# Kernel optimization log

Hardware: AMD Instinct MI355X
Metric: run time of the kernel (lower is better)

The kernel has to match this reference:

```python
import jax, jax.numpy as jnp
import numpy as np

GROUP_SIZE = 64
SCALING = 1.0  # lora_alpha / r = 16 / 16
# bitsandbytes NF4 codebook (16 normal-float levels)
NF4_CODE = jnp.array([
    -1.0, -0.6961928009986877, -0.5250730514526367, -0.39491748809814453,
    -0.28444138169288635, -0.18477343022823334, -0.09105003625154495, 0.0,
    0.07958029955625534, 0.16093020141124725, 0.24611230194568634,
    0.33791524171829224, 0.44070982933044434, 0.5626170039176941,
    0.7229568362236023, 1.0], dtype=jnp.float32)

IN_F, OUT_F, R, TOKENS = 4096, 11008, 16, 32


def setup_inputs() -> dict:
    key = jax.random.key(0)
    k0, k1, k2, k3, k4 = jax.random.split(key, 5)
    x = jax.random.normal(k0, (TOKENS, IN_F), dtype=jnp.float32)
    # each byte packs two 4-bit NF4 indices (high nibble first)
    packed_weight = jax.random.randint(k1, (OUT_F * IN_F // 2,), 0, 256, dtype=jnp.int32)
    # per-group absmax scales (positive)
    scales = jax.random.uniform(k2, (OUT_F * IN_F // GROUP_SIZE,), dtype=jnp.float32,
                                minval=0.005, maxval=0.05)
    lora_A = jax.random.normal(k3, (R, IN_F), dtype=jnp.float32) * 0.02
    lora_B = jax.random.normal(k4, (OUT_F, R), dtype=jnp.float32) * 0.02
    return {"x": x, "packed_weight": packed_weight, "scales": scales,
            "lora_A": lora_A, "lora_B": lora_B}


def _dequant_nf4(packed_weight, scales):
    hi = packed_weight // 16          # first nibble
    lo = packed_weight % 16           # second nibble
    idx = jnp.stack([hi, lo], axis=-1).reshape(-1)          # [out*in]
    w = NF4_CODE[idx].reshape(-1, GROUP_SIZE) * scales[:, None]
    return w.reshape(OUT_F, IN_F)                            # [out, in]


def reference(x, packed_weight, scales, lora_A, lora_B):
    W = _dequant_nf4(packed_weight, scales)
    base = x @ W.T                                           # [tokens, out]
    lora = (x @ lora_A.T) @ lora_B.T                         # low-rank update
    return base + SCALING * lora
```

## Files before the change

kernel.cpp:

```cpp
#include <hip/hip_runtime.h>
#include <hip/hip_bf16.h>

#define IN_F 4096
#define OUT_F 11008
#define TOKENS 32
#define RANK 16
#define KSPLIT 8
#define KSLICE (IN_F / KSPLIT)

typedef unsigned short u16;
typedef __attribute__((ext_vector_type(8))) short bf16x8;
typedef __attribute__((ext_vector_type(4))) float f32x4;

__device__ const float NF4_d[16] = {
    -1.0f, -0.6961928009986877f, -0.5250730514526367f, -0.39491748809814453f,
    -0.28444138169288635f, -0.18477343022823334f, -0.09105003625154495f, 0.0f,
    0.07958029955625534f, 0.16093020141124725f, 0.24611230194568634f,
    0.33791524171829224f, 0.44070982933044434f, 0.5626170039176941f,
    0.7229568362236023f, 1.0f};

static __device__ __forceinline__ unsigned pk2(float a, float b) {
    __hip_bfloat162 h = __float22bfloat162_rn(make_float2(a, b));
    unsigned u;
    __builtin_memcpy(&u, &h, 4);
    return u;
}

__global__ void cvt_x(const float* __restrict__ x, u16* __restrict__ xbf) {
    int i4 = blockIdx.x * 256 + threadIdx.x;
    float4 v = ((const float4*)x)[i4];
    uint2 o;
    o.x = pk2(v.x, v.y);
    o.y = pk2(v.z, v.w);
    ((uint2*)xbf)[i4] = o;
}

__global__ void lora_xa(const float* __restrict__ x, const float* __restrict__ A,
                        float* __restrict__ xa) {
    int b = blockIdx.x;
    int t = b >> 4, r = b & 15;
    const float4* xr = (const float4*)(x + t * IN_F);
    const float4* ar = (const float4*)(A + r * IN_F);
    float s = 0.f;
    for (int c = 0; c < 4; ++c) {
        int j = c * 256 + threadIdx.x;
        float4 xv = xr[j], av = ar[j];
        s += xv.x * av.x + xv.y * av.y + xv.z * av.z + xv.w * av.w;
    }
    __shared__ float red[256];
    red[threadIdx.x] = s;
    __syncthreads();
    for (int st = 128; st > 0; st >>= 1) {
        if (threadIdx.x < st) red[threadIdx.x] += red[threadIdx.x + st];
        __syncthreads();
    }
    if (threadIdx.x == 0) xa[b] = red[0];
}

__global__ void lora_out(const float* __restrict__ xa, const float* __restrict__ B,
                         float* __restrict__ out) {
    int idx = blockIdx.x * 256 + threadIdx.x;
    int t = idx / OUT_F;
    int o = idx - t * OUT_F;
    const float4* br = (const float4*)(B + o * RANK);
    const float4* xr = (const float4*)(xa + t * RANK);
    float acc = 0.f;
    for (int c = 0; c < 4; ++c) {
        float4 bv = br[c], xv = xr[c];
        acc += bv.x * xv.x + bv.y * xv.y + bv.z * xv.z + bv.w * xv.w;
    }
    out[idx] = acc;
}

__global__ __launch_bounds__(256) void qlora_main(const int* __restrict__ packed,
                                                  const float* __restrict__ scales,
                                                  const u16* __restrict__ xbf,
                                                  float* __restrict__ out) {
    __shared__ u16 xs[32 * 520];
    __shared__ float2 tbl[256];
    const int tid = threadIdx.x;
    const int kbase = blockIdx.y * KSLICE;

    tbl[tid] = make_float2(NF4_d[tid >> 4], NF4_d[tid & 15]);

    for (int it = 0; it < 8; ++it) {
        int row = it * 4 + (tid >> 6);
        int c8 = tid & 63;
        const uint4* src = (const uint4*)(xbf + row * IN_F + kbase + c8 * 8);
        *(uint4*)(xs + row * 520 + c8 * 8) = *src;
    }
    __syncthreads();

    const int lane = tid & 63;
    const int wv = tid >> 6;
    const int n = lane & 15;
    const int q = lane >> 4;
    const int o = blockIdx.x * 64 + wv * 16 + n;
    const int rowbase = o * 2048;

    f32x4 acc0 = {0.f, 0.f, 0.f, 0.f};
    f32x4 acc1 = {0.f, 0.f, 0.f, 0.f};
    const u16* xrow0 = xs + n * 520 + q * 8;
    const u16* xrow1 = xs + (n + 16) * 520 + q * 8;

    for (int kk = 0; kk < KSLICE; kk += 32) {
        int k = kbase + kk;
        int4 pw = *(const int4*)(packed + rowbase + (k >> 1) + q * 4);
        float s = scales[o * 64 + ((k + q * 8) >> 6)];

        float2 c0 = tbl[pw.x & 255];
        float2 c1 = tbl[pw.y & 255];
        float2 c2 = tbl[pw.z & 255];
        float2 c3 = tbl[pw.w & 255];
        uint4 bu;
        bu.x = pk2(c0.x * s, c0.y * s);
        bu.y = pk2(c1.x * s, c1.y * s);
        bu.z = pk2(c2.x * s, c2.y * s);
        bu.w = pk2(c3.x * s, c3.y * s);
        bf16x8 bfrag;
        __builtin_memcpy(&bfrag, &bu, 16);

        bf16x8 a0 = *(const bf16x8*)(xrow0 + kk);
        bf16x8 a1 = *(const bf16x8*)(xrow1 + kk);
        acc0 = __builtin_amdgcn_mfma_f32_16x16x32_bf16(a0, bfrag, acc0, 0, 0, 0);
        acc1 = __builtin_amdgcn_mfma_f32_16x16x32_bf16(a1, bfrag, acc1, 0, 0, 0);
    }

    for (int r = 0; r < 4; ++r) {
        int t = q * 4 + r;
        atomicAdd(out + t * OUT_F + o, acc0[r]);
        atomicAdd(out + (t + 16) * OUT_F + o, acc1[r]);
    }
}

extern "C" void kernel_launch(void* const* d_in, const int* in_sizes, int n_in,
                              void* d_out, int out_size, void* d_ws, size_t ws_size,
                              hipStream_t stream) {
    const float* x = (const float*)d_in[0];
    const int* packed = (const int*)d_in[1];
    const float* scales = (const float*)d_in[2];
    const float* lora_A = (const float*)d_in[3];
    const float* lora_B = (const float*)d_in[4];
    float* out = (float*)d_out;

    u16* xbf = (u16*)d_ws;
    float* xa = (float*)((char*)d_ws + TOKENS * IN_F * 2);

    cvt_x<<<128, 256, 0, stream>>>(x, xbf);
    lora_xa<<<512, 256, 0, stream>>>(x, lora_A, xa);
    lora_out<<<(TOKENS * OUT_F) / 256, 256, 0, stream>>>(xa, lora_B, out);
    qlora_main<<<dim3(OUT_F / 64, KSPLIT), 256, 0, stream>>>(packed, scales, xbf, out);
}
```

Baseline: 163.0 us.

## Prefetch packed weights, stage scales in LDS, and merge prep kernels

The main loop is fully unrolled and software-pipelined: the next two int4 weight chunks are loaded while the current two are dequantized and fed to MFMAs. Per-group scales for the block are loaded into shared memory once instead of read from global memory on each iteration. The x-to-bf16 conversion and x·A LoRA kernels are merged into a single launch with branch-selected roles. This targets global load latency in the memory-bound main kernel and one launch, at the cost of more registers and extra LDS.

```diff
diff --git a/kernel.cpp b/kernel.cpp
--- a/kernel.cpp
+++ b/kernel.cpp
@@ -7,6 +7,7 @@
 #define RANK 16
 #define KSPLIT 8
 #define KSLICE (IN_F / KSPLIT)
+#define XPAD 520
 
 typedef unsigned short u16;
 typedef __attribute__((ext_vector_type(8))) short bf16x8;
@@ -26,17 +27,18 @@
     return u;
 }
 
-__global__ void cvt_x(const float* __restrict__ x, u16* __restrict__ xbf) {
-    int i4 = blockIdx.x * 256 + threadIdx.x;
-    float4 v = ((const float4*)x)[i4];
-    uint2 o;
-    o.x = pk2(v.x, v.y);
-    o.y = pk2(v.z, v.w);
-    ((uint2*)xbf)[i4] = o;
-}
-
-__global__ void lora_xa(const float* __restrict__ x, const float* __restrict__ A,
-                        float* __restrict__ xa) {
+__global__ void prep(const float* __restrict__ x, const float* __restrict__ A,
+                     u16* __restrict__ xbf, float* __restrict__ xa) {
+    __shared__ float red[256];
+    if (blockIdx.x >= 512) {
+        int i4 = (blockIdx.x - 512) * 256 + threadIdx.x;
+        float4 v = ((const float4*)x)[i4];
+        uint2 o;
+        o.x = pk2(v.x, v.y);
+        o.y = pk2(v.z, v.w);
+        ((uint2*)xbf)[i4] = o;
+        return;
+    }
     int b = blockIdx.x;
     int t = b >> 4, r = b & 15;
     const float4* xr = (const float4*)(x + t * IN_F);
@@ -47,7 +49,6 @@
         float4 xv = xr[j], av = ar[j];
         s += xv.x * av.x + xv.y * av.y + xv.z * av.z + xv.w * av.w;
     }
-    __shared__ float red[256];
     red[threadIdx.x] = s;
     __syncthreads();
     for (int st = 128; st > 0; st >>= 1) {
@@ -76,18 +77,27 @@
                                                   const float* __restrict__ scales,
                                                   const u16* __restrict__ xbf,
                                                   float* __restrict__ out) {
-    __shared__ u16 xs[32 * 520];
+    __shared__ u16 xs[32 * XPAD];
     __shared__ float2 tbl[256];
+    __shared__ float sl[64 * 9];
     const int tid = threadIdx.x;
     const int kbase = blockIdx.y * KSLICE;
+    const int obase = blockIdx.x * 64;
 
     tbl[tid] = make_float2(NF4_d[tid >> 4], NF4_d[tid & 15]);
+
+    {
+        int r = tid >> 3, g = tid & 7;
+        int g0 = (kbase >> 6);
+        sl[r * 9 + g] = scales[(obase + r) * 64 + g0 + g];
+        sl[(r + 32) * 9 + g] = scales[(obase + r + 32) * 64 + g0 + g];
+    }
 
     for (int it = 0; it < 8; ++it) {
         int row = it * 4 + (tid >> 6);
         int c8 = tid & 63;
-        const uint4* src = (const uint4*)(xbf + row * IN_F + kbase + c8 * 8);
-        *(uint4*)(xs + row * 520 + c8 * 8) = *src;
+        *(uint4*)(xs + row * XPAD + c8 * 8) =
+            *(const uint4*)(xbf + row * IN_F + kbase + c8 * 8);
     }
     __syncthreads();
 
@@ -95,35 +105,64 @@
     const int wv = tid >> 6;
     const int n = lane & 15;
     const int q = lane >> 4;
-    const int o = blockIdx.x * 64 + wv * 16 + n;
-    const int rowbase = o * 2048;
+    const int o = obase + wv * 16 + n;
+
+    const int4* pp = (const int4*)(packed + o * 2048 + (kbase >> 1)) + q;
 
     f32x4 acc0 = {0.f, 0.f, 0.f, 0.f};
     f32x4 acc1 = {0.f, 0.f, 0.f, 0.f};
-    const u16* xrow0 = xs + n * 520 + q * 8;
-    const u16* xrow1 = xs + (n + 16) * 520 + q * 8;
+    const u16* xr0 = xs + n * XPAD + q * 8;
+    const u16* xr1 = xs + (n + 16) * XPAD + q * 8;
+    const float* slp = sl + (wv * 16 + n) * 9;
 
-    for (int kk = 0; kk < KSLICE; kk += 32) {
-        int k = kbase + kk;
-        int4 pw = *(const int4*)(packed + rowbase + (k >> 1) + q * 4);
-        float s = scales[o * 64 + ((k + q * 8) >> 6)];
+    int4 c0 = pp[0];
+    int4 c1 = pp[4];
 
-        float2 c0 = tbl[pw.x & 255];
-        float2 c1 = tbl[pw.y & 255];
-        float2 c2 = tbl[pw.z & 255];
-        float2 c3 = tbl[pw.w & 255];
-        uint4 bu;
-        bu.x = pk2(c0.x * s, c0.y * s);
-        bu.y = pk2(c1.x * s, c1.y * s);
-        bu.z = pk2(c2.x * s, c2.y * s);
-        bu.w = pk2(c3.x * s, c3.y * s);
-        bf16x8 bfrag;
-        __builtin_memcpy(&bfrag, &bu, 16);
+#pragma unroll
+    for (int s = 0; s < 16; s += 2) {
+        int4 n0 = c0, n1 = c1;
+        if (s + 2 < 16) {
+            n0 = pp[(s + 2) * 4];
+            n1 = pp[(s + 3) * 4];
+        }
+        float sc = slp[s >> 1];
 
-        bf16x8 a0 = *(const bf16x8*)(xrow0 + kk);
-        bf16x8 a1 = *(const bf16x8*)(xrow1 + kk);
-        acc0 = __builtin_amdgcn_mfma_f32_16x16x32_bf16(a0, bfrag, acc0, 0, 0, 0);
-        acc1 = __builtin_amdgcn_mfma_f32_16x16x32_bf16(a1, bfrag, acc1, 0, 0, 0);
+        {
+            float2 d0 = tbl[c0.x & 255];
+            float2 d1 = tbl[c0.y & 255];
+            float2 d2 = tbl[c0.z & 255];
+            float2 d3 = tbl[c0.w & 255];
+            uint4 bu;
+            bu.x = pk2(d0.x * sc, d0.y * sc);
+            bu.y = pk2(d1.x * sc, d1.y * sc);
+            bu.z = pk2(d2.x * sc, d2.y * sc);
+            bu.w = pk2(d3.x * sc, d3.y * sc);
+            bf16x8 bfrag;
+            __builtin_memcpy(&bfrag, &bu, 16);
+            bf16x8 a0 = *(const bf16x8*)(xr0 + s * 32);
+            bf16x8 a1 = *(const bf16x8*)(xr1 + s * 32);
+            acc0 = __builtin_amdgcn_mfma_f32_16x16x32_bf16(a0, bfrag, acc0, 0, 0, 0);
+            acc1 = __builtin_amdgcn_mfma_f32_16x16x32_bf16(a1, bfrag, acc1, 0, 0, 0);
+        }
+        {
+            float2 d0 = tbl[c1.x & 255];
+            float2 d1 = tbl[c1.y & 255];
+            float2 d2 = tbl[c1.z & 255];
+            float2 d3 = tbl[c1.w & 255];
+            uint4 bu;
+            bu.x = pk2(d0.x * sc, d0.y * sc);
+            bu.y = pk2(d1.x * sc, d1.y * sc);
+            bu.z = pk2(d2.x * sc, d2.y * sc);
+            bu.w = pk2(d3.x * sc, d3.y * sc);
+            bf16x8 bfrag;
+            __builtin_memcpy(&bfrag, &bu, 16);
+            bf16x8 a0 = *(const bf16x8*)(xr0 + (s + 1) * 32);
+            bf16x8 a1 = *(const bf16x8*)(xr1 + (s + 1) * 32);
+            acc0 = __builtin_amdgcn_mfma_f32_16x16x32_bf16(a0, bfrag, acc0, 0, 0, 0);
+            acc1 = __builtin_amdgcn_mfma_f32_16x16x32_bf16(a1, bfrag, acc1, 0, 0, 0);
+        }
+        c0 = n0;
+        c1 = n1;
     }
 
     for (int r = 0; r < 4; ++r) {
@@ -146,8 +185,7 @@
     u16* xbf = (u16*)d_ws;
     float* xa = (float*)((char*)d_ws + TOKENS * IN_F * 2);
 
-    cvt_x<<<128, 256, 0, stream>>>(x, xbf);
-    lora_xa<<<512, 256, 0, stream>>>(x, lora_A, xa);
+    prep<<<640, 256, 0, stream>>>(x, lora_A, xbf, xa);
     lora_out<<<(TOKENS * OUT_F) / 256, 256, 0, stream>>>(xa, lora_B, out);
     qlora_main<<<dim3(OUT_F / 64, KSPLIT), 256, 0, stream>>>(packed, scales, xbf, out);
 }
```

Result: faster. 155.6 us (-4.6%).
